# Kernel tuning notes

Measured on AMD Instinct MI355X. Metric: run time of the kernel, lower is better.

Reference implementation:

```python
import jax, jax.numpy as jnp
import numpy as np

SQRT2 = 1.4142135623730951
INV_SQRT_2PI = 0.3989422804014327

def Phi(x):
    # standard normal CDF
    return 0.5 * (1.0 + jax.lax.erf(x / SQRT2))

def phi(x):
    # standard normal pdf
    return INV_SQRT_2PI * jnp.exp(-0.5 * x * x)

def phip(x):
    # derivative of the standard normal pdf
    return -x * phi(x)


def setup_inputs() -> dict:
    key = jax.random.key(0)
    k1, k2, k3 = jax.random.split(key, 3)
    bs, n, c, d = 4, 256, 96, 2
    xin = jax.random.normal(k1, (bs, n, d), dtype=jnp.float32)
    meanin = jax.random.normal(k2, (bs, n, c), dtype=jnp.float32)
    # SPD spatial covariance: A A^T / n + 0.5 I (eigenvalues >> 1e-6)
    A = jax.random.normal(k3, (bs, n, n), dtype=jnp.float32)
    kin = A @ jnp.swapaxes(A, -1, -2) / n + 0.5 * jnp.eye(n, dtype=jnp.float32)
    return {"xin": xin, "meanin": meanin, "kin": kin}


def reference(xin, meanin, kin):
    bs, n, c = meanin.shape
    eye = jnp.eye(n, dtype=kin.dtype)
    kin = kin + eye * 1e-6
    kdiag = jnp.diagonal(kin, axis1=-2, axis2=-1)            # (bs,n)
    stdin = jnp.sqrt(jnp.clip(kdiag[..., None], 1e-8))       # (bs,n,1)
    z = meanin / stdin
    Phis = Phi(z)
    phis = phi(z)
    Eh = meanin * Phis + stdin * phis                        # (bs,n,c)

    # 2x2 matrix K12 per (i,j): [[k_ii, k_ij], [k_ji, k_jj]] -- kept as scalars
    m00 = kdiag[:, :, None]                                  # (bs,n,1) -> broadcast (bs,n,n)
    m11 = kdiag[:, None, :]
    m01 = kin
    m10 = jnp.swapaxes(kin, -1, -2)

    # matrix square root of 2x2 SPD: (M + sqrt(det) I) / sqrt(tr + 2 sqrt(det))
    det = m00 * m11 - m01 * m10
    tr = m00 + m11
    s = jnp.sqrt(jnp.clip(det, 1e-8))
    t = jnp.clip(jnp.sqrt(tr + 2.0 * s), 1e-8)
    s00 = (m00 + s) / t
    s01 = m01 / t
    s10 = m10 / t
    s11 = (m11 + s) / t

    # inverse of the 2x2 sqrt
    dS = jnp.clip(s00 * s11 - s01 * s10, 1e-8)
    i00 = s11 / dS
    i01 = -s01 / dS
    i10 = -s10 / dS
    i11 = s00 / dS

    mi = meanin[:, :, None, :]                               # (bs,n,1,c)
    mj = meanin[:, None, :, :]                               # (bs,1,n,c)

    u1 = i00[..., None] * mi + i01[..., None] * mj           # (bs,n,n,c)
    u2 = i10[..., None] * mi + i11[..., None] * mj
    Phi1 = Phi(u1)
    Phi2 = Phi(u2)
    p1 = phi(u1)
    p2 = phi(u2)

    Psi = Phi1 * Phi2
    psi1 = p1 * Phi2
    psi2 = Phi1 * p2

    EhhT_Psi = (mi * mj + kin[..., None]) * Psi
    EhhT_psi1 = (mj * s00[..., None] + mi * s10[..., None]) * psi1
    EhhT_psi2 = (mj * s01[..., None] + mi * s11[..., None]) * psi2

    SHPhiS11 = s00[..., None] * s01[..., None] * phip(u1) * Phi2
    SHPhiS12 = s01[..., None] * s01[..., None] * p1 * p2
    SHPhiS22 = s01[..., None] * s11[..., None] * Phi1 * phip(u2)
    SHPhiS = SHPhiS11 + 2.0 * SHPhiS12 + SHPhiS22

    EhhT = EhhT_Psi + (EhhT_psi1 + EhhT_psi2) + SHPhiS
    covar = (EhhT - Eh[:, :, None, :] * Eh[:, None, :, :]).mean(-1)   # (bs,n,n)

    dvals = jnp.clip(
        ((meanin ** 2 + stdin ** 2) * Phis + meanin * stdin * phis - Eh ** 2).mean(-1),
        1e-6,
    )                                                        # (bs,n)
    diag_covar = dvals[..., None] * eye                      # diag_embed
    full_covar = jnp.where(diag_covar > 1e-7, diag_covar, covar)
    return (xin, Eh, full_covar + eye * 1e-6)
```

## Files before the change

### kernel.cpp

```cpp
#include <hip/hip_runtime.h>
#include <math.h>

#define BSZ 4
#define NN  256
#define CC  96

#define XIN_OFF  0
#define EH_OFF   2048
#define COV_OFF  100352

#define INV_SQRT_2PI 0.3989422804014327f
#define INV_SQRT2    0.7071067811865476f
#define EXP2C       -0.7213475204444817f

__device__ __forceinline__ float phi_cdf_from_exp(float u, float e) {
    float x = fabsf(u) * INV_SQRT2;
    float t = __builtin_amdgcn_rcpf(__builtin_fmaf(0.3275911f, x, 1.0f));
    float poly = __builtin_fmaf(__builtin_fmaf(__builtin_fmaf(__builtin_fmaf(
                     0.5307027145f, t, -0.7265760135f), t, 0.7107068705f), t,
                     -0.142248368f), t, 0.127414796f) * t;
    float hp = poly * e;
    return (u >= 0.0f) ? 1.0f - hp : hp;
}

__global__ __launch_bounds__(128) void relu_cov_row(
    const float* __restrict__ xin, const float* __restrict__ meanin,
    const float* __restrict__ kin, float* __restrict__ out)
{
    const int row = blockIdx.x;
    const int b   = row >> 8;
    const int i   = row & (NN - 1);
    const int tid = threadIdx.x;

    const float kd   = kin[((size_t)b * NN + i) * NN + i] + 1e-6f;
    const float var  = fmaxf(kd, 1e-8f);
    const float stdv = __builtin_amdgcn_sqrtf(var);
    const float rstd = __builtin_amdgcn_rcpf(stdv);

    float dterm = 0.0f;
    if (tid < CC) {
        float m  = meanin[(size_t)row * CC + tid];
        float z  = m * rstd;
        float e  = __builtin_amdgcn_exp2f(z * z * EXP2C);
        float ph = INV_SQRT_2PI * e;
        float Ph = phi_cdf_from_exp(z, e);
        float Eh = m * Ph + stdv * ph;
        out[EH_OFF + (size_t)row * CC + tid] = Eh;
        dterm = (m * m + var) * Ph + m * stdv * ph - Eh * Eh;
    } else if (tid < CC + 2) {
        int dd = tid - CC;
        out[XIN_OFF + (size_t)row * 2 + dd] = xin[(size_t)row * 2 + dd];
    }

    float v = dterm;
    v += __shfl_down(v, 32, 64);
    v += __shfl_down(v, 16, 64);
    v += __shfl_down(v,  8, 64);
    v += __shfl_down(v,  4, 64);
    v += __shfl_down(v,  2, 64);
    v += __shfl_down(v,  1, 64);
    __shared__ float wsum[2];
    if ((tid & 63) == 0) wsum[tid >> 6] = v;
    __syncthreads();
    if (tid == 0) {
        float dval = fmaxf((wsum[0] + wsum[1]) * (1.0f / 96.0f), 1e-6f);
        out[COV_OFF + ((size_t)b * NN + i) * NN + i] = dval + 1e-6f;
    }
}

__global__ __launch_bounds__(1024, 8) void relu_cov_pair(
    const float* __restrict__ meanin, const float* __restrict__ kin,
    float* __restrict__ out)
{
    const int blk = blockIdx.x;
    const int b   = blk >> 7;
    const int i2  = blk & 127;
    const int tid = threadIdx.x;
    const int p   = tid & 255;
    const int ch  = tid >> 8;

    __shared__ __align__(16) float smA[CC], sEA[CC], smB[CC], sEB[CC];
    __shared__ float red[1024];

    const float* __restrict__ Eh = out + EH_OFF;
    const int rowA = i2;
    const int rowB = 255 - i2;

    if (tid < CC) {
        smA[tid] = meanin[((size_t)b * NN + rowA) * CC + tid];
        sEA[tid] = Eh[((size_t)b * NN + rowA) * CC + tid];
    } else if (tid >= 128 && tid < 128 + CC) {
        int c = tid - 128;
        smB[c] = meanin[((size_t)b * NN + rowB) * CC + c];
        sEB[c] = Eh[((size_t)b * NN + rowB) * CC + c];
    }
    __syncthreads();

    const int  nfirst   = 255 - i2;
    const bool firstSeg = p < nfirst;
    const bool active   = p < 255;
    const int  i = firstSeg ? rowA : rowB;
    const int  j = firstSeg ? (i2 + 1 + p) : (p + 1);

    float acc = 0.0f;
    int iw = i, jw = j;
    if (active) {
        const float* kb = kin + (size_t)b * NN * NN;
        const float m00 = kb[i * NN + i] + 1e-6f;
        const float m11 = kb[j * NN + j] + 1e-6f;
        const float m01 = 0.5f * (kb[i * NN + j] + kb[j * NN + i]);

        const float det = __builtin_fmaf(-m01, m01, m00 * m11);
        const float s   = __builtin_amdgcn_sqrtf(fmaxf(det, 1e-8f));
        const float t   = fmaxf(__builtin_amdgcn_sqrtf(m00 + m11 + 2.0f * s), 1e-8f);
        const float rt  = __builtin_amdgcn_rcpf(t);
        const float s00 = (m00 + s) * rt;
        const float s01 = m01 * rt;
        const float s11 = (m11 + s) * rt;
        const float dS  = fmaxf(__builtin_fmaf(-s01, s01, s00 * s11), 1e-8f);
        const float rdS = __builtin_amdgcn_rcpf(dS);
        const float i00 = s11 * rdS;
        const float i01 = -s01 * rdS;
        const float i11 = s00 * rdS;
        const float c0001   = s00 * s01;
        const float c0101_2 = 2.0f * s01 * s01;
        const float c0111   = s01 * s11;

        const float4* mjp = (const float4*)(meanin + ((size_t)b * NN + j) * CC + ch * 24);
        const float4* Ejp = (const float4*)(Eh     + ((size_t)b * NN + j) * CC + ch * 24);
        const float4* mip = (const float4*)((firstSeg ? smA : smB) + ch * 24);
        const float4* Eip = (const float4*)((firstSeg ? sEA : sEB) + ch * 24);

        auto elem = [&](float mi, float mj, float Ehi, float Ehj) {
            float u1 = __builtin_fmaf(i01, mj, i00 * mi);
            float u2 = __builtin_fmaf(i11, mj, i01 * mi);
            float e1 = __builtin_amdgcn_exp2f(u1 * u1 * EXP2C);
            float e2 = __builtin_amdgcn_exp2f(u2 * u2 * EXP2C);
            float p1 = INV_SQRT_2PI * e1;
            float p2 = INV_SQRT_2PI * e2;
            float Phi1 = phi_cdf_from_exp(u1, e1);
            float Phi2 = phi_cdf_from_exp(u2, e2);
            float a  = __builtin_fmaf(mi, mj, m01);
            float bb = __builtin_fmaf(mi, s01, mj * s00);
            bb = __builtin_fmaf(-c0001, u1, bb);
            float g1 = __builtin_fmaf(bb, p1, a * Phi1);
            float cc = __builtin_fmaf(mi, s11, mj * s01);
            cc = __builtin_fmaf(-c0111, u2, cc);
            float g2 = cc * p2;
            acc = __builtin_fmaf(Phi2, g1, acc);
            acc = __builtin_fmaf(Phi1, g2, acc);
            acc = __builtin_fmaf(c0101_2, p1 * p2, acc);
            acc = __builtin_fmaf(-Ehi, Ehj, acc);
        };

#pragma unroll 2
        for (int q = 0; q < 6; ++q) {
            float4 mj4 = mjp[q];
            float4 Ej4 = Ejp[q];
            float4 mi4 = mip[q];
            float4 Ei4 = Eip[q];
            elem(mi4.x, mj4.x, Ei4.x, Ej4.x);
            elem(mi4.y, mj4.y, Ei4.y, Ej4.y);
            elem(mi4.z, mj4.z, Ei4.z, Ej4.z);
            elem(mi4.w, mj4.w, Ei4.w, Ej4.w);
        }
    }

    red[tid] = acc;
    __syncthreads();

    if (tid < 256 && active) {
        float v = red[tid] + red[tid + 256] + red[tid + 512] + red[tid + 768];
        v *= (1.0f / 96.0f);
        out[COV_OFF + (((size_t)b * NN + iw) * NN + jw)] = v;
        out[COV_OFF + (((size_t)b * NN + jw) * NN + iw)] = v;
    }
}

extern "C" void kernel_launch(void* const* d_in, const int* in_sizes, int n_in,
                              void* d_out, int out_size, void* d_ws, size_t ws_size,
                              hipStream_t stream) {
    const float* xin    = (const float*)d_in[0];
    const float* meanin = (const float*)d_in[1];
    const float* kin    = (const float*)d_in[2];
    float* out = (float*)d_out;

    relu_cov_row<<<BSZ * NN, 128, 0, stream>>>(xin, meanin, kin, out);
    relu_cov_pair<<<BSZ * 128, 1024, 0, stream>>>(meanin, kin, out);
}
```

Baseline: 88.95 us.

## Use cheaper normal CDF approximation, packed-float math, and split channel reduction across blocks

Replaces the 5-term erf approximation with a shorter 3-coefficient rational form, and rewrites the pair kernel to use two-wide float vectors so the compiler can emit packed FP32 ops. The 1024-thread block with in-block shared-memory reduction is split into four 256-thread blocks per row pair, one per channel chunk. A new combine kernel sums the partials from workspace and writes the symmetric output. This adds a kernel launch and workspace traffic, and the shorter approximation may lose accuracy.

Result: slower. 93.51 us (+5.1%).

```diff
diff --git a/kernel.cpp b/kernel.cpp
--- a/kernel.cpp
+++ b/kernel.cpp
@@ -10,17 +10,50 @@
 #define COV_OFF  100352
 
 #define INV_SQRT_2PI 0.3989422804014327f
-#define INV_SQRT2    0.7071067811865476f
 #define EXP2C       -0.7213475204444817f
-
-__device__ __forceinline__ float phi_cdf_from_exp(float u, float e) {
-    float x = fabsf(u) * INV_SQRT2;
-    float t = __builtin_amdgcn_rcpf(__builtin_fmaf(0.3275911f, x, 1.0f));
-    float poly = __builtin_fmaf(__builtin_fmaf(__builtin_fmaf(__builtin_fmaf(
-                     0.5307027145f, t, -0.7265760135f), t, 0.7107068705f), t,
-                     -0.142248368f), t, 0.127414796f) * t;
-    float hp = poly * e;
-    return (u >= 0.0f) ? 1.0f - hp : hp;
+#define PHI_P   0.33267253f
+#define PHI_C1  0.1740121f
+#define PHI_C2 -0.0479399f
+#define PHI_C3  0.3739278f
+
+typedef float        v2f __attribute__((ext_vector_type(2)));
+typedef unsigned int v2u __attribute__((ext_vector_type(2)));
+
+__device__ __forceinline__ v2f v2s(float s) { v2f r; r.x = s; r.y = s; return r; }
+
+#if __has_builtin(__builtin_elementwise_fma)
+#define V2FMA(a, b, c) __builtin_elementwise_fma((a), (b), (c))
+#else
+#define V2FMA(a, b, c) ((a) * (b) + (c))
+#endif
+
+__device__ __forceinline__ v2f v2_exp2(v2f x) {
+    v2f r; r.x = __builtin_amdgcn_exp2f(x.x); r.y = __builtin_amdgcn_exp2f(x.y);
+    return r;
+}
+__device__ __forceinline__ v2f v2_rcp(v2f x) {
+    v2f r; r.x = __builtin_amdgcn_rcpf(x.x); r.y = __builtin_amdgcn_rcpf(x.y);
+    return r;
+}
+__device__ __forceinline__ v2f v2_abs(v2f x) {
+    v2u u = __builtin_bit_cast(v2u, x) & 0x7fffffffu;
+    return __builtin_bit_cast(v2f, u);
+}
+__device__ __forceinline__ v2f v2_copysign(v2f mag, v2f sgn) {
+    v2u m = __builtin_bit_cast(v2u, mag) & 0x7fffffffu;
+    v2u s = __builtin_bit_cast(v2u, sgn) & 0x80000000u;
+    return __builtin_bit_cast(v2f, m | s);
+}
+__device__ __forceinline__ v2f v2_phi_from_exp(v2f u, v2f e) {
+    v2f t  = v2_rcp(V2FMA(v2s(PHI_P), v2_abs(u), v2s(1.0f)));
+    v2f hp = V2FMA(V2FMA(v2s(PHI_C3), t, v2s(PHI_C2)), t, v2s(PHI_C1)) * t * e;
+    return v2s(0.5f) + v2_copysign(v2s(0.5f) - hp, u);
+}
+
+__device__ __forceinline__ float phi_from_exp_s(float u, float e) {
+    float t  = __builtin_amdgcn_rcpf(__builtin_fmaf(PHI_P, fabsf(u), 1.0f));
+    float hp = __builtin_fmaf(__builtin_fmaf(PHI_C3, t, PHI_C2), t, PHI_C1) * t * e;
+    return 0.5f + __builtin_copysignf(0.5f - hp, u);
 }
 
 __global__ __launch_bounds__(128) void relu_cov_row(
@@ -43,7 +76,7 @@
         float z  = m * rstd;
         float e  = __builtin_amdgcn_exp2f(z * z * EXP2C);
         float ph = INV_SQRT_2PI * e;
-        float Ph = phi_cdf_from_exp(z, e);
+        float Ph = phi_from_exp_s(z, e);
         float Eh = m * Ph + stdv * ph;
         out[EH_OFF + (size_t)row * CC + tid] = Eh;
         dterm = (m * m + var) * Ph + m * stdv * ph - Eh * Eh;
@@ -68,113 +101,124 @@
     }
 }
 
-__global__ __launch_bounds__(1024, 8) void relu_cov_pair(
+__global__ __launch_bounds__(256) void relu_cov_pair(
     const float* __restrict__ meanin, const float* __restrict__ kin,
-    float* __restrict__ out)
+    const float* __restrict__ Eh, float* __restrict__ partial)
 {
     const int blk = blockIdx.x;
     const int b   = blk >> 7;
     const int i2  = blk & 127;
-    const int tid = threadIdx.x;
-    const int p   = tid & 255;
-    const int ch  = tid >> 8;
-
-    __shared__ __align__(16) float smA[CC], sEA[CC], smB[CC], sEB[CC];
-    __shared__ float red[1024];
-
-    const float* __restrict__ Eh = out + EH_OFF;
+    const int ch  = blockIdx.y;
+    const int p   = threadIdx.x;
+
     const int rowA = i2;
     const int rowB = 255 - i2;
 
-    if (tid < CC) {
-        smA[tid] = meanin[((size_t)b * NN + rowA) * CC + tid];
-        sEA[tid] = Eh[((size_t)b * NN + rowA) * CC + tid];
-    } else if (tid >= 128 && tid < 128 + CC) {
-        int c = tid - 128;
-        smB[c] = meanin[((size_t)b * NN + rowB) * CC + c];
-        sEB[c] = Eh[((size_t)b * NN + rowB) * CC + c];
+    __shared__ __align__(16) float smA[24], sEA[24], smB[24], sEB[24];
+    {
+        const float* mA = meanin + ((size_t)(b * NN + rowA)) * CC + ch * 24;
+        const float* eA = Eh     + ((size_t)(b * NN + rowA)) * CC + ch * 24;
+        const float* mB = meanin + ((size_t)(b * NN + rowB)) * CC + ch * 24;
+        const float* eB = Eh     + ((size_t)(b * NN + rowB)) * CC + ch * 24;
+        if      (p < 24) smA[p]      = mA[p];
+        else if (p < 48) sEA[p - 24] = eA[p - 24];
+        else if (p < 72) smB[p - 48] = mB[p - 48];
+        else if (p < 96) sEB[p - 72] = eB[p - 72];
     }
     __syncthreads();
+
+    float* pout = partial + ((size_t)blk * 4 + ch) * 256 + p;
+    if (p >= 255) { *pout = 0.0f; return; }
 
     const int  nfirst   = 255 - i2;
     const bool firstSeg = p < nfirst;
-    const bool active   = p < 255;
     const int  i = firstSeg ? rowA : rowB;
     const int  j = firstSeg ? (i2 + 1 + p) : (p + 1);
 
-    float acc = 0.0f;
-    int iw = i, jw = j;
-    if (active) {
-        const float* kb = kin + (size_t)b * NN * NN;
-        const float m00 = kb[i * NN + i] + 1e-6f;
-        const float m11 = kb[j * NN + j] + 1e-6f;
-        const float m01 = 0.5f * (kb[i * NN + j] + kb[j * NN + i]);
-
-        const float det = __builtin_fmaf(-m01, m01, m00 * m11);
-        const float s   = __builtin_amdgcn_sqrtf(fmaxf(det, 1e-8f));
-        const float t   = fmaxf(__builtin_amdgcn_sqrtf(m00 + m11 + 2.0f * s), 1e-8f);
-        const float rt  = __builtin_amdgcn_rcpf(t);
-        const float s00 = (m00 + s) * rt;
-        const float s01 = m01 * rt;
-        const float s11 = (m11 + s) * rt;
-        const float dS  = fmaxf(__builtin_fmaf(-s01, s01, s00 * s11), 1e-8f);
-        const float rdS = __builtin_amdgcn_rcpf(dS);
-        const float i00 = s11 * rdS;
-        const float i01 = -s01 * rdS;
-        const float i11 = s00 * rdS;
-        const float c0001   = s00 * s01;
-        const float c0101_2 = 2.0f * s01 * s01;
-        const float c0111   = s01 * s11;
-
-        const float4* mjp = (const float4*)(meanin + ((size_t)b * NN + j) * CC + ch * 24);
-        const float4* Ejp = (const float4*)(Eh     + ((size_t)b * NN + j) * CC + ch * 24);
-        const float4* mip = (const float4*)((firstSeg ? smA : smB) + ch * 24);
-        const float4* Eip = (const float4*)((firstSeg ? sEA : sEB) + ch * 24);
-
-        auto elem = [&](float mi, float mj, float Ehi, float Ehj) {
-            float u1 = __builtin_fmaf(i01, mj, i00 * mi);
-            float u2 = __builtin_fmaf(i11, mj, i01 * mi);
-            float e1 = __builtin_amdgcn_exp2f(u1 * u1 * EXP2C);
-            float e2 = __builtin_amdgcn_exp2f(u2 * u2 * EXP2C);
-            float p1 = INV_SQRT_2PI * e1;
-            float p2 = INV_SQRT_2PI * e2;
-            float Phi1 = phi_cdf_from_exp(u1, e1);
-            float Phi2 = phi_cdf_from_exp(u2, e2);
-            float a  = __builtin_fmaf(mi, mj, m01);
-            float bb = __builtin_fmaf(mi, s01, mj * s00);
-            bb = __builtin_fmaf(-c0001, u1, bb);
-            float g1 = __builtin_fmaf(bb, p1, a * Phi1);
-            float cc = __builtin_fmaf(mi, s11, mj * s01);
-            cc = __builtin_fmaf(-c0111, u2, cc);
-            float g2 = cc * p2;
-            acc = __builtin_fmaf(Phi2, g1, acc);
-            acc = __builtin_fmaf(Phi1, g2, acc);
-            acc = __builtin_fmaf(c0101_2, p1 * p2, acc);
-            acc = __builtin_fmaf(-Ehi, Ehj, acc);
-        };
-
-#pragma unroll 2
-        for (int q = 0; q < 6; ++q) {
-            float4 mj4 = mjp[q];
-            float4 Ej4 = Ejp[q];
-            float4 mi4 = mip[q];
-            float4 Ei4 = Eip[q];
-            elem(mi4.x, mj4.x, Ei4.x, Ej4.x);
-            elem(mi4.y, mj4.y, Ei4.y, Ej4.y);
-            elem(mi4.z, mj4.z, Ei4.z, Ej4.z);
-            elem(mi4.w, mj4.w, Ei4.w, Ej4.w);
-        }
-    }
-
-    red[tid] = acc;
-    __syncthreads();
-
-    if (tid < 256 && active) {
-        float v = red[tid] + red[tid + 256] + red[tid + 512] + red[tid + 768];
-        v *= (1.0f / 96.0f);
-        out[COV_OFF + (((size_t)b * NN + iw) * NN + jw)] = v;
-        out[COV_OFF + (((size_t)b * NN + jw) * NN + iw)] = v;
-    }
+    const float* kb = kin + (size_t)b * NN * NN;
+    const float m00 = kb[i * NN + i] + 1e-6f;
+    const float m11 = kb[j * NN + j] + 1e-6f;
+    const float m01 = 0.5f * (kb[i * NN + j] + kb[j * NN + i]);
+
+    const float det = __builtin_fmaf(-m01, m01, m00 * m11);
+    const float s   = __builtin_amdgcn_sqrtf(fmaxf(det, 1e-8f));
+    const float t   = fmaxf(__builtin_amdgcn_sqrtf(m00 + m11 + 2.0f * s), 1e-8f);
+    const float rt  = __builtin_amdgcn_rcpf(t);
+    const float s00 = (m00 + s) * rt;
+    const float s01 = m01 * rt;
+    const float s11 = (m11 + s) * rt;
+    const float dS  = fmaxf(__builtin_fmaf(-s01, s01, s00 * s11), 1e-8f);
+    const float rdS = __builtin_amdgcn_rcpf(dS);
+    const float i00 = s11 * rdS;
+    const float i01 = -s01 * rdS;
+    const float i11 = s00 * rdS;
+    const float c0001   = s00 * s01;
+    const float c0101_2 = 2.0f * s01 * s01;
+    const float c0111   = s01 * s11;
+
+    const float4* mjp = (const float4*)(meanin + ((size_t)(b * NN + j)) * CC + ch * 24);
+    const float4* Ejp = (const float4*)(Eh     + ((size_t)(b * NN + j)) * CC + ch * 24);
+    const float4* mip = (const float4*)(firstSeg ? smA : smB);
+    const float4* Eip = (const float4*)(firstSeg ? sEA : sEB);
+
+    v2f acc0 = v2s(0.0f), acc1 = v2s(0.0f);
+
+    auto elem2 = [&](v2f mi, v2f mj, v2f Ei, v2f Ej) -> v2f {
+        v2f u1 = V2FMA(mj, v2s(i01), mi * i00);
+        v2f u2 = V2FMA(mj, v2s(i11), mi * i01);
+        v2f e1 = v2_exp2(u1 * u1 * EXP2C);
+        v2f e2 = v2_exp2(u2 * u2 * EXP2C);
+        v2f Phi1 = v2_phi_from_exp(u1, e1);
+        v2f Phi2 = v2_phi_from_exp(u2, e2);
+        v2f p1 = e1 * INV_SQRT_2PI;
+        v2f p2 = e2 * INV_SQRT_2PI;
+        v2f a  = V2FMA(mi, mj, v2s(m01));
+        v2f bb = V2FMA(mi, v2s(s01), mj * s00);
+        bb     = V2FMA(u1, v2s(-c0001), bb);
+        v2f g1 = V2FMA(bb, p1, a * Phi1);
+        v2f cc = V2FMA(mi, v2s(s11), mj * s01);
+        cc     = V2FMA(u2, v2s(-c0111), cc);
+        v2f r  = V2FMA(p1 * p2, v2s(c0101_2), Ei * (-Ej));
+        r      = V2FMA(Phi1, cc * p2, r);
+        r      = V2FMA(Phi2, g1, r);
+        return r;
+    };
+
+#pragma unroll
+    for (int q = 0; q < 6; ++q) {
+        float4 mj4 = mjp[q];
+        float4 Ej4 = Ejp[q];
+        float4 mi4 = mip[q];
+        float4 Ei4 = Eip[q];
+        v2f miL = {mi4.x, mi4.y}, miH = {mi4.z, mi4.w};
+        v2f mjL = {mj4.x, mj4.y}, mjH = {mj4.z, mj4.w};
+        v2f EiL = {Ei4.x, Ei4.y}, EiH = {Ei4.z, Ei4.w};
+        v2f EjL = {Ej4.x, Ej4.y}, EjH = {Ej4.z, Ej4.w};
+        acc0 += elem2(miL, mjL, EiL, EjL);
+        acc1 += elem2(miH, mjH, EiH, EjH);
+    }
+
+    v2f acc = acc0 + acc1;
+    *pout = acc.x + acc.y;
+}
+
+__global__ __launch_bounds__(256) void relu_cov_combine(
+    const float* __restrict__ partial, float* __restrict__ out)
+{
+    const int blk = blockIdx.x;
+    const int b   = blk >> 7;
+    const int i2  = blk & 127;
+    const int p   = threadIdx.x;
+    if (p >= 255) return;
+
+    const float* base = partial + ((size_t)blk * 4) * 256 + p;
+    float v = (base[0] + base[256] + base[512] + base[768]) * (1.0f / 96.0f);
+
+    const int nfirst = 255 - i2;
+    const int i = (p < nfirst) ? i2 : (255 - i2);
+    const int j = (p < nfirst) ? (i2 + 1 + p) : (p + 1);
+    out[COV_OFF + ((size_t)(b * NN + i)) * NN + j] = v;
+    out[COV_OFF + ((size_t)(b * NN + j)) * NN + i] = v;
 }
 
 extern "C" void kernel_launch(void* const* d_in, const int* in_sizes, int n_in,
@@ -183,8 +227,11 @@
     const float* xin    = (const float*)d_in[0];
     const float* meanin = (const float*)d_in[1];
     const float* kin    = (const float*)d_in[2];
-    float* out = (float*)d_out;
+    float* out     = (float*)d_out;
+    float* partial = (float*)d_ws;
 
     relu_cov_row<<<BSZ * NN, 128, 0, stream>>>(xin, meanin, kin, out);
-    relu_cov_pair<<<BSZ * 128, 1024, 0, stream>>>(meanin, kin, out);
-}
+    relu_cov_pair<<<dim3(BSZ * 128, 4), 256, 0, stream>>>(
+        meanin, kin, out + EH_OFF, partial);
+    relu_cov_combine<<<BSZ * 128, 256, 0, stream>>>(partial, out);
+}
```

## Use cheaper normal CDF approximation, shared reciprocal, and folded pair algebra

Applied to the files above, without the earlier changes.

Replaces the 5-term erf approximation with a 3-term polynomial form and computes both CDF reciprocals with a single rcp, cutting transcendental and FMA work per element. The psi/phip terms are algebraically folded into precomputed coefficients qd/qj/qi, and m01 is read from one side of the matrix instead of averaging both. The pair kernel now uses 512 threads with each thread covering 48 channels across two accumulators, and the launch bounds change accordingly. The lower-order CDF approximation reduces accuracy, and the single-sided m01 read assumes kin is symmetric.

New measurement: 85.10 us. 4.3% less time.

```diff
diff --git a/kernel.cpp b/kernel.cpp
--- a/kernel.cpp
+++ b/kernel.cpp
@@ -10,17 +10,16 @@
 #define COV_OFF  100352
 
 #define INV_SQRT_2PI 0.3989422804014327f
-#define INV_SQRT2    0.7071067811865476f
 #define EXP2C       -0.7213475204444817f
+#define PHI_P   0.33267253f
+#define PHI_C1  0.1740121f
+#define PHI_C2 -0.0479399f
+#define PHI_C3  0.3739278f
 
-__device__ __forceinline__ float phi_cdf_from_exp(float u, float e) {
-    float x = fabsf(u) * INV_SQRT2;
-    float t = __builtin_amdgcn_rcpf(__builtin_fmaf(0.3275911f, x, 1.0f));
-    float poly = __builtin_fmaf(__builtin_fmaf(__builtin_fmaf(__builtin_fmaf(
-                     0.5307027145f, t, -0.7265760135f), t, 0.7107068705f), t,
-                     -0.142248368f), t, 0.127414796f) * t;
-    float hp = poly * e;
-    return (u >= 0.0f) ? 1.0f - hp : hp;
+__device__ __forceinline__ float phi_from_exp_s(float u, float e) {
+    float t  = __builtin_amdgcn_rcpf(__builtin_fmaf(PHI_P, fabsf(u), 1.0f));
+    float hp = __builtin_fmaf(__builtin_fmaf(PHI_C3, t, PHI_C2), t, PHI_C1) * t * e;
+    return 0.5f + __builtin_copysignf(0.5f - hp, u);
 }
 
 __global__ __launch_bounds__(128) void relu_cov_row(
@@ -43,7 +42,7 @@
         float z  = m * rstd;
         float e  = __builtin_amdgcn_exp2f(z * z * EXP2C);
         float ph = INV_SQRT_2PI * e;
-        float Ph = phi_cdf_from_exp(z, e);
+        float Ph = phi_from_exp_s(z, e);
         float Eh = m * Ph + stdv * ph;
         out[EH_OFF + (size_t)row * CC + tid] = Eh;
         dterm = (m * m + var) * Ph + m * stdv * ph - Eh * Eh;
@@ -68,47 +67,45 @@
     }
 }
 
-__global__ __launch_bounds__(1024, 8) void relu_cov_pair(
+__global__ __launch_bounds__(512, 4) void relu_cov_pair(
     const float* __restrict__ meanin, const float* __restrict__ kin,
-    float* __restrict__ out)
+    const float* __restrict__ Eh, float* __restrict__ out)
 {
     const int blk = blockIdx.x;
     const int b   = blk >> 7;
     const int i2  = blk & 127;
     const int tid = threadIdx.x;
     const int p   = tid & 255;
-    const int ch  = tid >> 8;
+    const int h   = tid >> 8;
 
-    __shared__ __align__(16) float smA[CC], sEA[CC], smB[CC], sEB[CC];
-    __shared__ float red[1024];
-
-    const float* __restrict__ Eh = out + EH_OFF;
     const int rowA = i2;
     const int rowB = 255 - i2;
 
-    if (tid < CC) {
-        smA[tid] = meanin[((size_t)b * NN + rowA) * CC + tid];
-        sEA[tid] = Eh[((size_t)b * NN + rowA) * CC + tid];
-    } else if (tid >= 128 && tid < 128 + CC) {
-        int c = tid - 128;
-        smB[c] = meanin[((size_t)b * NN + rowB) * CC + c];
-        sEB[c] = Eh[((size_t)b * NN + rowB) * CC + c];
+    __shared__ __align__(16) float smA[CC], sEA[CC], smB[CC], sEB[CC];
+    __shared__ float red[512];
+    {
+        const float* mA = meanin + ((size_t)(b * NN + rowA)) * CC;
+        const float* eA = Eh     + ((size_t)(b * NN + rowA)) * CC;
+        const float* mB = meanin + ((size_t)(b * NN + rowB)) * CC;
+        const float* eB = Eh     + ((size_t)(b * NN + rowB)) * CC;
+        if      (tid < 96)  smA[tid]       = mA[tid];
+        else if (tid < 192) sEA[tid - 96]  = eA[tid - 96];
+        else if (tid < 288) smB[tid - 192] = mB[tid - 192];
+        else if (tid < 384) sEB[tid - 288] = eB[tid - 288];
     }
     __syncthreads();
 
-    const int  nfirst   = 255 - i2;
-    const bool firstSeg = p < nfirst;
-    const bool active   = p < 255;
-    const int  i = firstSeg ? rowA : rowB;
-    const int  j = firstSeg ? (i2 + 1 + p) : (p + 1);
+    float acc0 = 0.0f, acc1 = 0.0f;
+    if (p < 255) {
+        const int  nfirst   = 255 - i2;
+        const bool firstSeg = p < nfirst;
+        const int  i = firstSeg ? rowA : rowB;
+        const int  j = firstSeg ? (i2 + 1 + p) : (p + 1);
 
-    float acc = 0.0f;
-    int iw = i, jw = j;
-    if (active) {
-        const float* kb = kin + (size_t)b * NN * NN;
-        const float m00 = kb[i * NN + i] + 1e-6f;
-        const float m11 = kb[j * NN + j] + 1e-6f;
-        const float m01 = 0.5f * (kb[i * NN + j] + kb[j * NN + i]);
+        const float* kb  = kin + (size_t)b * NN * NN;
+        const float  m00 = kb[i * (NN + 1)] + 1e-6f;
+        const float  m11 = kb[j * (NN + 1)] + 1e-6f;
+        const float  m01 = kb[i * NN + j];
 
         const float det = __builtin_fmaf(-m01, m01, m00 * m11);
         const float s   = __builtin_amdgcn_sqrtf(fmaxf(det, 1e-8f));
@@ -122,58 +119,65 @@
         const float i00 = s11 * rdS;
         const float i01 = -s01 * rdS;
         const float i11 = s00 * rdS;
-        const float c0001   = s00 * s01;
-        const float c0101_2 = 2.0f * s01 * s01;
-        const float c0111   = s01 * s11;
+        const float qd = -s01 * s01 * s01 * rdS;
+        const float qj = s00 * s00 * s11 * rdS;
+        const float qi = s00 * s11 * s11 * rdS;
+        const float c2 = 2.0f * s01 * s01;
 
-        const float4* mjp = (const float4*)(meanin + ((size_t)b * NN + j) * CC + ch * 24);
-        const float4* Ejp = (const float4*)(Eh     + ((size_t)b * NN + j) * CC + ch * 24);
-        const float4* mip = (const float4*)((firstSeg ? smA : smB) + ch * 24);
-        const float4* Eip = (const float4*)((firstSeg ? sEA : sEB) + ch * 24);
+        const float4* mjp = (const float4*)(meanin + ((size_t)(b * NN + j)) * CC + h * 48);
+        const float4* Ejp = (const float4*)(Eh     + ((size_t)(b * NN + j)) * CC + h * 48);
+        const float4* mip = (const float4*)((firstSeg ? smA : smB) + h * 48);
+        const float4* Eip = (const float4*)((firstSeg ? sEA : sEB) + h * 48);
 
-        auto elem = [&](float mi, float mj, float Ehi, float Ehj) {
-            float u1 = __builtin_fmaf(i01, mj, i00 * mi);
-            float u2 = __builtin_fmaf(i11, mj, i01 * mi);
+        auto elem = [&](float mi, float mjv, float Ei, float Ej, float& acc) {
+            float u1 = __builtin_fmaf(i01, mjv, i00 * mi);
+            float u2 = __builtin_fmaf(i11, mjv, i01 * mi);
             float e1 = __builtin_amdgcn_exp2f(u1 * u1 * EXP2C);
             float e2 = __builtin_amdgcn_exp2f(u2 * u2 * EXP2C);
+            float d1 = __builtin_fmaf(PHI_P, fabsf(u1), 1.0f);
+            float d2 = __builtin_fmaf(PHI_P, fabsf(u2), 1.0f);
+            float rp = __builtin_amdgcn_rcpf(d1 * d2);
+            float t1 = d2 * rp;
+            float t2 = d1 * rp;
+            float hp1 = __builtin_fmaf(__builtin_fmaf(PHI_C3, t1, PHI_C2), t1, PHI_C1) * t1 * e1;
+            float hp2 = __builtin_fmaf(__builtin_fmaf(PHI_C3, t2, PHI_C2), t2, PHI_C1) * t2 * e2;
+            float Phi1 = 0.5f + __builtin_copysignf(0.5f - hp1, u1);
+            float Phi2 = 0.5f + __builtin_copysignf(0.5f - hp2, u2);
             float p1 = INV_SQRT_2PI * e1;
             float p2 = INV_SQRT_2PI * e2;
-            float Phi1 = phi_cdf_from_exp(u1, e1);
-            float Phi2 = phi_cdf_from_exp(u2, e2);
-            float a  = __builtin_fmaf(mi, mj, m01);
-            float bb = __builtin_fmaf(mi, s01, mj * s00);
-            bb = __builtin_fmaf(-c0001, u1, bb);
-            float g1 = __builtin_fmaf(bb, p1, a * Phi1);
-            float cc = __builtin_fmaf(mi, s11, mj * s01);
-            cc = __builtin_fmaf(-c0111, u2, cc);
-            float g2 = cc * p2;
-            acc = __builtin_fmaf(Phi2, g1, acc);
-            acc = __builtin_fmaf(Phi1, g2, acc);
-            acc = __builtin_fmaf(c0101_2, p1 * p2, acc);
-            acc = __builtin_fmaf(-Ehi, Ehj, acc);
+            float a  = __builtin_fmaf(mi, mjv, m01);
+            float bb = __builtin_fmaf(qd, mi, qj * mjv);
+            float cc = __builtin_fmaf(qi, mi, qd * mjv);
+            acc = __builtin_fmaf(a,  Phi1 * Phi2, acc);
+            acc = __builtin_fmaf(bb, p1 * Phi2,  acc);
+            acc = __builtin_fmaf(cc, Phi1 * p2,  acc);
+            acc = __builtin_fmaf(c2, p1 * p2,    acc);
+            acc = __builtin_fmaf(-Ei, Ej,        acc);
         };
 
-#pragma unroll 2
-        for (int q = 0; q < 6; ++q) {
+#pragma unroll 3
+        for (int q = 0; q < 12; ++q) {
             float4 mj4 = mjp[q];
             float4 Ej4 = Ejp[q];
             float4 mi4 = mip[q];
             float4 Ei4 = Eip[q];
-            elem(mi4.x, mj4.x, Ei4.x, Ej4.x);
-            elem(mi4.y, mj4.y, Ei4.y, Ej4.y);
-            elem(mi4.z, mj4.z, Ei4.z, Ej4.z);
-            elem(mi4.w, mj4.w, Ei4.w, Ej4.w);
+            elem(mi4.x, mj4.x, Ei4.x, Ej4.x, acc0);
+            elem(mi4.y, mj4.y, Ei4.y, Ej4.y, acc1);
+            elem(mi4.z, mj4.z, Ei4.z, Ej4.z, acc0);
+            elem(mi4.w, mj4.w, Ei4.w, Ej4.w, acc1);
         }
     }
 
-    red[tid] = acc;
+    red[tid] = acc0 + acc1;
     __syncthreads();
 
-    if (tid < 256 && active) {
-        float v = red[tid] + red[tid + 256] + red[tid + 512] + red[tid + 768];
-        v *= (1.0f / 96.0f);
-        out[COV_OFF + (((size_t)b * NN + iw) * NN + jw)] = v;
-        out[COV_OFF + (((size_t)b * NN + jw) * NN + iw)] = v;
+    if (tid < 255) {
+        float v = (red[tid] + red[tid + 256]) * (1.0f / 96.0f);
+        const int nfirst = 255 - i2;
+        const int i = (tid < nfirst) ? i2 : (255 - i2);
+        const int j = (tid < nfirst) ? (i2 + 1 + tid) : (tid + 1);
+        out[COV_OFF + ((size_t)(b * NN + i)) * NN + j] = v;
+        out[COV_OFF + ((size_t)(b * NN + j)) * NN + i] = v;
     }
 }
 
@@ -186,5 +190,5 @@
     float* out = (float*)d_out;
 
     relu_cov_row<<<BSZ * NN, 128, 0, stream>>>(xin, meanin, kin, out);
-    relu_cov_pair<<<BSZ * 128, 1024, 0, stream>>>(meanin, kin, out);
+    relu_cov_pair<<<BSZ * 128, 512, 0, stream>>>(meanin, kin, out + EH_OFF, out);
 }
```
